# Optimization experiments

Hardware: AMD Instinct MI355X
Metric: run time of the kernel (lower is better)

## Reference

```python
import jax, jax.numpy as jnp
import numpy as np

N_EMBD = 768
N_HEAD = 12


def setup_inputs() -> dict:
    key = jax.random.key(0)
    ks = jax.random.split(key, 5)
    B, T, C = 8, 1024, N_EMBD
    s_in = 1.0 / np.sqrt(C)
    x = jax.random.normal(ks[0], (B, T, C), dtype=jnp.float32)
    w_attn = jax.random.normal(ks[1], (C, 3 * C), dtype=jnp.float32) * s_in
    b_attn = jnp.zeros((3 * C,), dtype=jnp.float32)
    w_proj = jax.random.normal(ks[2], (C, C), dtype=jnp.float32) * s_in
    b_proj = jnp.zeros((C,), dtype=jnp.float32)
    return {"x": x, "w_attn": w_attn, "b_attn": b_attn,
            "w_proj": w_proj, "b_proj": b_proj}


def reference(x, w_attn, b_attn, w_proj, b_proj):
    B, T, C = x.shape
    H, hs = N_HEAD, C // N_HEAD
    qkv = x @ w_attn + b_attn                      # [B,T,3C]
    q, k, v = jnp.split(qkv, 3, axis=-1)
    # [B,H,T,hs]
    q = q.reshape(B, T, H, hs).transpose(0, 2, 1, 3)
    k = k.reshape(B, T, H, hs).transpose(0, 2, 1, 3)
    v = v.reshape(B, T, H, hs).transpose(0, 2, 1, 3)
    att = jnp.einsum('bhqd,bhkd->bhqk', q, k) * (1.0 / np.sqrt(hs))
    causal = jnp.tril(jnp.ones((T, T), dtype=bool))
    att = jnp.where(causal, att, -jnp.inf)
    att = jax.nn.softmax(att, axis=-1)
    y = jnp.einsum('bhqk,bhkd->bhqd', att, v)      # [B,H,T,hs]
    y = y.transpose(0, 2, 1, 3).reshape(B, T, C)
    return y @ w_proj + b_proj
```

## Files before the change

kernel.cpp:

```cpp
#include <hip/hip_runtime.h>
#include <hip/hip_bf16.h>
#include <stdint.h>

typedef unsigned short u16;
typedef short short8 __attribute__((ext_vector_type(8)));
typedef short short4v __attribute__((ext_vector_type(4)));
typedef float floatx4 __attribute__((ext_vector_type(4)));

__device__ __forceinline__ float b2f(u16 v) {
  union { unsigned int u; float f; } c; c.u = ((unsigned int)v) << 16; return c.f;
}
__device__ __forceinline__ u16 f2b(float f) {
  union { float f; unsigned int u; } c; c.f = f;
  unsigned int u = c.u;
  return (u16)((u + 0x7fffu + ((u >> 16) & 1u)) >> 16);
}

__device__ __forceinline__ void gld_lds16(const u16* g, u16* l) {
  __builtin_amdgcn_global_load_lds(
      (const __attribute__((address_space(1))) unsigned int*)g,
      (__attribute__((address_space(3))) unsigned int*)l,
      16, 0, 0);
}

__device__ __forceinline__ void tile_transpose_f2b(
    const float* __restrict__ in, u16* __restrict__ out,
    int inRS, int outRS, int rb, int cb, int tid)
{
  __shared__ __align__(16) u16 t[64][72];
  const int r = tid >> 2, sg = tid & 3;
  const float* ip = in + (long)(rb + r) * inRS + cb + sg * 16;
#pragma unroll
  for (int i = 0; i < 16; i += 4) {
    float4 f = *(const float4*)(ip + i);
    t[r][sg * 16 + i]     = f2b(f.x);
    t[r][sg * 16 + i + 1] = f2b(f.y);
    t[r][sg * 16 + i + 2] = f2b(f.z);
    t[r][sg * 16 + i + 3] = f2b(f.w);
  }
  __syncthreads();
  short8 v0, v1;
#pragma unroll
  for (int i = 0; i < 8; i++) v0[i] = (short)t[sg * 16 + i][r];
#pragma unroll
  for (int i = 0; i < 8; i++) v1[i] = (short)t[sg * 16 + 8 + i][r];
  *(short8*)(out + (long)(cb + r) * outRS + rb + sg * 16)     = v0;
  *(short8*)(out + (long)(cb + r) * outRS + rb + sg * 16 + 8) = v1;
}

__global__ __launch_bounds__(256) void prep(
    const float* __restrict__ x, u16* __restrict__ xb,
    const float* __restrict__ w_attn, u16* __restrict__ wTa,
    const float* __restrict__ w_proj, u16* __restrict__ wTp)
{
  const int bid = blockIdx.x, tid = threadIdx.x;
  if (bid < 6144) {
    int i = (bid * 256 + tid) * 4;
    float4 f = *(const float4*)(x + i);
    short4v v;
    v[0] = (short)f2b(f.x); v[1] = (short)f2b(f.y);
    v[2] = (short)f2b(f.z); v[3] = (short)f2b(f.w);
    *(short4v*)(xb + i) = v;
  } else if (bid < 6576) {
    int t = bid - 6144;
    tile_transpose_f2b(w_attn, wTa, 2304, 768, (t / 36) * 64, (t % 36) * 64, tid);
  } else {
    int t = bid - 6576;
    tile_transpose_f2b(w_proj, wTp, 768, 768, (t / 12) * 64, (t % 12) * 64, tid);
  }
}

__device__ __forceinline__ void store_out(u16* p, float v)  { *p = f2b(v); }
__device__ __forceinline__ void store_out(float* p, float v) { *p = v; }

template <int BM>
__device__ __forceinline__ void stage(
    const u16* __restrict__ A, const u16* __restrict__ Bt,
    long rowbase, long colbase, int K, int k0,
    u16* dA, u16* dB, int tid)
{
  const int c0 = tid, c1 = tid + 256;
  const int ar0 = c0 >> 2, ak0 = (c0 & 3) * 8;
  const int ar1 = c1 >> 2, ak1 = (c1 & 3) * 8;
  gld_lds16(A + (rowbase + ar0) * K + k0 + ak0, dA + c0 * 8);
  if (BM == 128)
    gld_lds16(A + (rowbase + ar1) * K + k0 + ak1, dA + c1 * 8);
  gld_lds16(Bt + (colbase + ar0) * K + k0 + ak0, dB + c0 * 8);
  gld_lds16(Bt + (colbase + ar1) * K + k0 + ak1, dB + c1 * 8);
}

template <typename OT, int BM, bool SPLIT>
__global__ __launch_bounds__(256) void gemm_bt_bias(
    const u16* __restrict__ A, const u16* __restrict__ Bt,
    const float* __restrict__ bias, OT* __restrict__ C, u16* __restrict__ vT,
    int M, int N, int K, int strideC)
{
  constexpr int WNF = (BM == 128) ? 4 : 2;
  __shared__ __align__(16) u16 sA[2][BM * 32];
  __shared__ __align__(16) u16 sB[2][128 * 32];
  const int tid = threadIdx.x;
  const int lane = tid & 63;
  const int wave = tid >> 6;
  const int wm = (BM == 128) ? (wave >> 1) * 64 : 0;
  const int wn = (BM == 128) ? (wave & 1) * 64 : wave * 32;
  const int l15 = lane & 15;
  const int q = lane >> 4;
  const long rowbase = (long)blockIdx.y * BM;
  const long colbase = (long)blockIdx.x * 128;

  floatx4 acc[4][WNF];
#pragma unroll
  for (int i = 0; i < 4; i++)
#pragma unroll
    for (int j = 0; j < WNF; j++) acc[i][j] = (floatx4){0.f, 0.f, 0.f, 0.f};

  stage<BM>(A, Bt, rowbase, colbase, K, 0, sA[0], sB[0], tid);
  __syncthreads();

  const int NIT = K / 32;
  for (int it = 0; it < NIT; ++it) {
    const int cur = it & 1;
    if (it + 1 < NIT)
      stage<BM>(A, Bt, rowbase, colbase, K, (it + 1) * 32, sA[cur ^ 1], sB[cur ^ 1], tid);
    short8 af[4], bf[WNF];
#pragma unroll
    for (int mt = 0; mt < 4; mt++)
      af[mt] = *(const short8*)(sA[cur] + (wm + mt * 16 + l15) * 32 + q * 8);
#pragma unroll
    for (int nt = 0; nt < WNF; nt++)
      bf[nt] = *(const short8*)(sB[cur] + (wn + nt * 16 + l15) * 32 + q * 8);
#pragma unroll
    for (int mt = 0; mt < 4; mt++)
#pragma unroll
      for (int nt = 0; nt < WNF; nt++)
        acc[mt][nt] = __builtin_amdgcn_mfma_f32_16x16x32_bf16(af[mt], bf[nt], acc[mt][nt], 0, 0, 0);
    if (it + 1 < NIT) __syncthreads();
  }

  if (SPLIT && colbase >= 1536) {
    const long b = rowbase >> 10;
    const int t0b = (int)(rowbase & 1023) + wm;
#pragma unroll
    for (int nt = 0; nt < WNF; nt++) {
      const int col = (int)colbase + wn + nt * 16 + l15;
      const float bv = bias[col];
      const int dloc = col - 1536;
      u16* bp = vT + (b * 12 + (dloc >> 6)) * 65536L + (long)(dloc & 63) * 1024;
#pragma unroll
      for (int mt = 0; mt < 4; mt++) {
        short4v pv;
#pragma unroll
        for (int r = 0; r < 4; r++) pv[r] = (short)f2b(acc[mt][nt][r] + bv);
        *(short4v*)(bp + t0b + mt * 16 + q * 4) = pv;
      }
    }
  } else {
#pragma unroll
    for (int nt = 0; nt < WNF; nt++) {
      const long col = colbase + wn + nt * 16 + l15;
      const float bv = bias[col];
#pragma unroll
      for (int mt = 0; mt < 4; mt++)
#pragma unroll
        for (int r = 0; r < 4; r++) {
          const long row = rowbase + wm + mt * 16 + q * 4 + r;
          store_out(C + row * strideC + col, acc[mt][nt][r] + bv);
        }
    }
  }
}

#define QKV_K 768
#define QKV_NT 24
#define VMW(n) asm volatile("s_waitcnt vmcnt(" #n ")" ::: "memory")

__global__ __launch_bounds__(768, 3) void gemm_qkv_288(
    const u16* __restrict__ A, const u16* __restrict__ Bt,
    const float* __restrict__ bias, u16* __restrict__ qkOut, u16* __restrict__ vT)
{
  __shared__ __align__(16) u16 sA[4][256 * 32];
  __shared__ __align__(16) u16 sB[4][288 * 32];

  const int bid = blockIdx.x;
  const int wg = (bid & 7) * 32 + (bid >> 3);
  const int bx = wg & 7;
  const int by = wg >> 3;

  const int tid = threadIdx.x;
  const int lane = tid & 63;
  const int l15 = lane & 15, q = lane >> 4;
  const int wave = tid >> 6;
  const int wm = (wave / 6) * 128;
  const int wn = (wave % 6) * 48;
  const long rowbase = (long)by * 256;
  const long colbase = (long)bx * 288;
  const int xq = ((q ^ ((l15 >> 1) & 3)) << 3);

  const int cA0 = tid, cA1 = 768 + tid;
  const int cB0 = tid, cB1 = 768 + tid;
  const u16* pa0 = A + (rowbase + (cA0 >> 2)) * QKV_K + ((((cA0 & 3) ^ ((cA0 >> 3) & 3))) << 3);
  const u16* pa1 = A + (rowbase + (cA1 >> 2)) * QKV_K + ((((cA1 & 3) ^ ((cA1 >> 3) & 3))) << 3);
  const u16* pb0 = Bt + (colbase + (cB0 >> 2)) * QKV_K + ((((cB0 & 3) ^ ((cB0 >> 3) & 3))) << 3);
  const u16* pb1 = Bt + (colbase + (cB1 >> 2)) * QKV_K + ((((cB1 & 3) ^ ((cB1 >> 3) & 3))) << 3);
  const bool hasA1 = (tid < 256);
  const bool hasB1 = (tid < 384);

#define STAGE(t, s) do { \
    const long k0_ = (long)(t) * 32; \
    gld_lds16(pa0 + k0_, &sA[s][cA0 * 8]); \
    if (hasA1) gld_lds16(pa1 + k0_, &sA[s][cA1 * 8]); \
    gld_lds16(pb0 + k0_, &sB[s][cB0 * 8]); \
    if (hasB1) gld_lds16(pb1 + k0_, &sB[s][cB1 * 8]); } while (0)

  floatx4 acc[8][3];
#pragma unroll
  for (int i = 0; i < 8; i++)
#pragma unroll
    for (int n = 0; n < 3; n++) acc[i][n] = (floatx4){0.f, 0.f, 0.f, 0.f};

  STAGE(0, 0); STAGE(1, 1); STAGE(2, 2);
  if (wave < 4) VMW(8); else if (wave < 6) VMW(6); else VMW(4);
  __builtin_amdgcn_s_barrier();

#pragma unroll 4
  for (int j = 0; j < QKV_NT; ++j) {
    const int slot = j & 3;
    const u16* ap = sA[slot];
    const u16* bp = sB[slot];

    short8 bf[3];
#pragma unroll
    for (int nt = 0; nt < 3; nt++)
      bf[nt] = *(const short8*)(bp + (wn + nt * 16 + l15) * 32 + xq);
    short8 af[4];
#pragma unroll
    for (int mt = 0; mt < 4; mt++)
      af[mt] = *(const short8*)(ap + (wm + mt * 16 + l15) * 32 + xq);
    if (j + 3 < QKV_NT) STAGE(j + 3, (j + 3) & 3);
    __builtin_amdgcn_s_setprio(1);
#pragma unroll
    for (int mt = 0; mt < 4; mt++)
#pragma unroll
      for (int nt = 0; nt < 3; nt++)
        acc[mt][nt] = __builtin_amdgcn_mfma_f32_16x16x32_bf16(af[mt], bf[nt], acc[mt][nt], 0, 0, 0);
    __builtin_amdgcn_s_setprio(0);

#pragma unroll
    for (int mt = 0; mt < 4; mt++)
      af[mt] = *(const short8*)(ap + (wm + 64 + mt * 16 + l15) * 32 + xq);
    __builtin_amdgcn_s_setprio(1);
#pragma unroll
    for (int mt = 0; mt < 4; mt++)
#pragma unroll
      for (int nt = 0; nt < 3; nt++)
        acc[4 + mt][nt] = __builtin_amdgcn_mfma_f32_16x16x32_bf16(af[mt], bf[nt], acc[4 + mt][nt], 0, 0, 0);
    __builtin_amdgcn_s_setprio(0);

    if (j < QKV_NT - 1) {
      if (j + 3 < QKV_NT) {
        if (wave < 4) VMW(8); else if (wave < 6) VMW(6); else VMW(4);
      } else if (j + 2 < QKV_NT) {
        if (wave < 4) VMW(4); else if (wave < 6) VMW(3); else VMW(2);
      } else {
        VMW(0);
      }
      __builtin_amdgcn_s_barrier();
    }
  }
#undef STAGE

#pragma unroll
  for (int nt = 0; nt < 3; nt++) {
    const int fragc = (int)colbase + wn + nt * 16;
    const int col = fragc + l15;
    const float bv = bias[col];
    if (fragc >= 1536) {
      const long bb = rowbase >> 10;
      const int dloc = col - 1536;
      u16* op = vT + (bb * 12 + (dloc >> 6)) * 65536L + (long)(dloc & 63) * 1024;
      const int t0 = (int)(rowbase & 1023) + wm;
#pragma unroll
      for (int mt = 0; mt < 8; mt++) {
        short4v pv;
#pragma unroll
        for (int r = 0; r < 4; r++) pv[r] = (short)f2b(acc[mt][nt][r] + bv);
        *(short4v*)(op + t0 + mt * 16 + q * 4) = pv;
      }
    } else {
#pragma unroll
      for (int mt = 0; mt < 8; mt++)
#pragma unroll
        for (int r = 0; r < 4; r++) {
          const long row = rowbase + wm + mt * 16 + q * 4 + r;
          qkOut[row * 1536 + col] = f2b(acc[mt][nt][r] + bv);
        }
    }
  }
}
#undef VMW

__global__ __launch_bounds__(512) void attn_fwd(
    const u16* __restrict__ qk, const u16* __restrict__ vT, u16* __restrict__ y)
{
  const int bh = blockIdx.x;
  const int qt = 7 - blockIdx.y;
  const int b = bh / 12, h = bh % 12;
  const long rowOff = (long)b * 1024;
  const int qb = qt * 128;

  __shared__ __align__(16) u16 sK[64 * 72];
  __shared__ __align__(16) u16 sV[2][64 * 72];
  __shared__ __align__(16) u16 sP[128 * 72];

  const int tid = threadIdx.x;
  const int lane = tid & 63, wave = tid >> 6;
  const int l15 = lane & 15, q = lane >> 4;
  const int qrow_l = wave * 16 + l15;
  const int qrow_g = qb + qrow_l;
  const int wave_max_row = qb + wave * 16 + 15;

  const int sr = tid >> 3, sc = (tid & 7) * 8;
  const u16* kBase = qk + rowOff * 1536 + 768 + (long)h * 64;
  const u16* vBase = vT + (long)bh * 65536;

  short8 qf[2];
  {
    const u16* qp = qk + (long)(rowOff + qrow_g) * 1536 + h * 64 + q * 8;
    short8 a0 = *(const short8*)(qp);
    short8 a1 = *(const short8*)(qp + 32);
#pragma unroll
    for (int i = 0; i < 8; i++) {
      a0[i] = (short)f2b(b2f((u16)a0[i]) * 0.125f);
      a1[i] = (short)f2b(b2f((u16)a1[i]) * 0.125f);
    }
    qf[0] = a0; qf[1] = a1;
  }

  float m_i = -1e30f, l_i = 0.f;
  floatx4 o[4];
#pragma unroll
  for (int nt = 0; nt < 4; nt++) o[nt] = (floatx4){0.f, 0.f, 0.f, 0.f};

  const int J = 2 * qt + 1;

  *(short8*)(sK + sr * 72 + sc)    = *(const short8*)(kBase + (long)sr * 1536 + sc);
  *(short8*)(sV[0] + sr * 72 + sc) = *(const short8*)(vBase + (long)sr * 1024 + sc);
  __syncthreads();

  for (int j = 0; j <= J; j++) {
    const int jb = j * 64;
    const bool active = (jb <= wave_max_row);
    const u16* sVc = sV[j & 1];

    short8 rk = {}, rv = {};
    if (j < J) {
      rk = *(const short8*)(kBase + (long)(jb + 64 + sr) * 1536 + sc);
      rv = *(const short8*)(vBase + (long)sr * 1024 + (jb + 64) + sc);
    }

    float al = 1.f;
    if (active) {
      floatx4 sf[4];
#pragma unroll
      for (int mt = 0; mt < 4; mt++) sf[mt] = (floatx4){0.f, 0.f, 0.f, 0.f};
#pragma unroll
      for (int kk = 0; kk < 2; kk++) {
#pragma unroll
        for (int mt = 0; mt < 4; mt++) {
          short8 kf = *(const short8*)(sK + (mt * 16 + l15) * 72 + kk * 32 + q * 8);
          sf[mt] = __builtin_amdgcn_mfma_f32_16x16x32_bf16(kf, qf[kk], sf[mt], 0, 0, 0);
        }
      }

      float mx = m_i;
#pragma unroll
      for (int mt = 0; mt < 4; mt++)
#pragma unroll
        for (int r = 0; r < 4; r++) {
          int key_g = jb + mt * 16 + q * 4 + r;
          float v = sf[mt][r];
          if (key_g > qrow_g) v = -1e30f;
          sf[mt][r] = v;
          mx = fmaxf(mx, v);
        }
      mx = fmaxf(mx, __shfl_xor(mx, 16));
      mx = fmaxf(mx, __shfl_xor(mx, 32));
      al = __expf(m_i - mx);
      m_i = mx;
      float rsum = 0.f;
#pragma unroll
      for (int mt = 0; mt < 4; mt++) {
        short4v pv;
#pragma unroll
        for (int r = 0; r < 4; r++) {
          float p = __expf(sf[mt][r] - mx);
          rsum += p;
          pv[r] = (short)f2b(p);
        }
        *(short4v*)(sP + qrow_l * 72 + mt * 16 + q * 4) = pv;
      }
      rsum += __shfl_xor(rsum, 16);
      rsum += __shfl_xor(rsum, 32);
      l_i = l_i * al + rsum;
    }
    __syncthreads();

    if (j < J) {
      *(short8*)(sK + sr * 72 + sc)            = rk;
      *(short8*)(sV[(j + 1) & 1] + sr * 72 + sc) = rv;
    }

    if (active) {
      float al_r[4];
#pragma unroll
      for (int r = 0; r < 4; r++) al_r[r] = __shfl(al, q * 4 + r);
#pragma unroll
      for (int nt = 0; nt < 4; nt++)
#pragma unroll
        for (int r = 0; r < 4; r++) o[nt][r] *= al_r[r];
#pragma unroll
      for (int kk = 0; kk < 2; kk++) {
        short8 pf = *(const short8*)(sP + qrow_l * 72 + kk * 32 + q * 8);
#pragma unroll
        for (int nt = 0; nt < 4; nt++) {
          short8 vf = *(const short8*)(sVc + (nt * 16 + l15) * 72 + kk * 32 + q * 8);
          o[nt] = __builtin_amdgcn_mfma_f32_16x16x32_bf16(pf, vf, o[nt], 0, 0, 0);
        }
      }
    }
    __syncthreads();
  }

  float linv = 1.f / l_i;
  float li_r[4];
#pragma unroll
  for (int r = 0; r < 4; r++) li_r[r] = __shfl(linv, q * 4 + r);
#pragma unroll
  for (int nt = 0; nt < 4; nt++)
#pragma unroll
    for (int r = 0; r < 4; r++) {
      int row = qb + wave * 16 + q * 4 + r;
      int col = h * 64 + nt * 16 + l15;
      y[(rowOff + row) * 768 + col] = f2b(o[nt][r] * li_r[r]);
    }
}

extern "C" void kernel_launch(void* const* d_in, const int* in_sizes, int n_in,
                              void* d_out, int out_size, void* d_ws, size_t ws_size,
                              hipStream_t stream) {
  const float* x      = (const float*)d_in[0];
  const float* w_attn = (const float*)d_in[1];
  const float* b_attn = (const float*)d_in[2];
  const float* w_proj = (const float*)d_in[3];
  const float* b_proj = (const float*)d_in[4];
  float* out = (float*)d_out;

  char* ws = (char*)d_ws;
  u16* xb   = (u16*)ws; ws += (size_t)8192 * 768 * 2;
  u16* wTa  = (u16*)ws; ws += (size_t)2304 * 768 * 2;
  u16* wTp  = (u16*)ws; ws += (size_t)768 * 768 * 2;
  u16* qk   = (u16*)ws; ws += (size_t)8192 * 1536 * 2;
  u16* vT   = (u16*)ws; ws += (size_t)96 * 64 * 1024 * 2;
  u16* yatt = (u16*)ws; ws += (size_t)8192 * 768 * 2;

  prep<<<dim3(6720), 256, 0, stream>>>(x, xb, w_attn, wTa, w_proj, wTp);

  gemm_qkv_288<<<dim3(256), 768, 0, stream>>>(xb, wTa, b_attn, qk, vT);

  attn_fwd<<<dim3(96, 8), 512, 0, stream>>>(qk, vT, yatt);

  gemm_bt_bias<float, 128, false><<<dim3(6, 64), 256, 0, stream>>>(
      yatt, wTp, b_proj, out, (u16*)nullptr, 8192, 768, 768, 768);
}
```

Baseline: 188.8 us.

## Unify QKV and projection GEMMs into templated 3-stage pipelined kernel

Replaces the 256x288 QKV GEMM (768 threads, 4-stage) with a templated 128xBN kernel using 384 threads and a 3-stage cp.async-style LDS pipeline with swizzled layout. The output projection GEMM also moves from the simple double-buffered 128x128 kernel onto this pipelined kernel with 128x96 tiles and 512 blocks. The aim is better occupancy and grid fill for the QKV GEMM and better latency hiding for the projection GEMM. Smaller tiles lower data reuse per block, and the shallower pipeline may hide less memory latency.

```diff
diff --git a/kernel.cpp b/kernel.cpp
--- a/kernel.cpp
+++ b/kernel.cpp
@@ -73,116 +73,23 @@
 __device__ __forceinline__ void store_out(u16* p, float v)  { *p = f2b(v); }
 __device__ __forceinline__ void store_out(float* p, float v) { *p = v; }
 
-template <int BM>
-__device__ __forceinline__ void stage(
-    const u16* __restrict__ A, const u16* __restrict__ Bt,
-    long rowbase, long colbase, int K, int k0,
-    u16* dA, u16* dB, int tid)
-{
-  const int c0 = tid, c1 = tid + 256;
-  const int ar0 = c0 >> 2, ak0 = (c0 & 3) * 8;
-  const int ar1 = c1 >> 2, ak1 = (c1 & 3) * 8;
-  gld_lds16(A + (rowbase + ar0) * K + k0 + ak0, dA + c0 * 8);
-  if (BM == 128)
-    gld_lds16(A + (rowbase + ar1) * K + k0 + ak1, dA + c1 * 8);
-  gld_lds16(Bt + (colbase + ar0) * K + k0 + ak0, dB + c0 * 8);
-  gld_lds16(Bt + (colbase + ar1) * K + k0 + ak1, dB + c1 * 8);
-}
-
-template <typename OT, int BM, bool SPLIT>
-__global__ __launch_bounds__(256) void gemm_bt_bias(
-    const u16* __restrict__ A, const u16* __restrict__ Bt,
-    const float* __restrict__ bias, OT* __restrict__ C, u16* __restrict__ vT,
-    int M, int N, int K, int strideC)
-{
-  constexpr int WNF = (BM == 128) ? 4 : 2;
-  __shared__ __align__(16) u16 sA[2][BM * 32];
-  __shared__ __align__(16) u16 sB[2][128 * 32];
-  const int tid = threadIdx.x;
-  const int lane = tid & 63;
-  const int wave = tid >> 6;
-  const int wm = (BM == 128) ? (wave >> 1) * 64 : 0;
-  const int wn = (BM == 128) ? (wave & 1) * 64 : wave * 32;
-  const int l15 = lane & 15;
-  const int q = lane >> 4;
-  const long rowbase = (long)blockIdx.y * BM;
-  const long colbase = (long)blockIdx.x * 128;
-
-  floatx4 acc[4][WNF];
-#pragma unroll
-  for (int i = 0; i < 4; i++)
-#pragma unroll
-    for (int j = 0; j < WNF; j++) acc[i][j] = (floatx4){0.f, 0.f, 0.f, 0.f};
-
-  stage<BM>(A, Bt, rowbase, colbase, K, 0, sA[0], sB[0], tid);
-  __syncthreads();
-
-  const int NIT = K / 32;
-  for (int it = 0; it < NIT; ++it) {
-    const int cur = it & 1;
-    if (it + 1 < NIT)
-      stage<BM>(A, Bt, rowbase, colbase, K, (it + 1) * 32, sA[cur ^ 1], sB[cur ^ 1], tid);
-    short8 af[4], bf[WNF];
-#pragma unroll
-    for (int mt = 0; mt < 4; mt++)
-      af[mt] = *(const short8*)(sA[cur] + (wm + mt * 16 + l15) * 32 + q * 8);
-#pragma unroll
-    for (int nt = 0; nt < WNF; nt++)
-      bf[nt] = *(const short8*)(sB[cur] + (wn + nt * 16 + l15) * 32 + q * 8);
-#pragma unroll
-    for (int mt = 0; mt < 4; mt++)
-#pragma unroll
-      for (int nt = 0; nt < WNF; nt++)
-        acc[mt][nt] = __builtin_amdgcn_mfma_f32_16x16x32_bf16(af[mt], bf[nt], acc[mt][nt], 0, 0, 0);
-    if (it + 1 < NIT) __syncthreads();
-  }
-
-  if (SPLIT && colbase >= 1536) {
-    const long b = rowbase >> 10;
-    const int t0b = (int)(rowbase & 1023) + wm;
-#pragma unroll
-    for (int nt = 0; nt < WNF; nt++) {
-      const int col = (int)colbase + wn + nt * 16 + l15;
-      const float bv = bias[col];
-      const int dloc = col - 1536;
-      u16* bp = vT + (b * 12 + (dloc >> 6)) * 65536L + (long)(dloc & 63) * 1024;
-#pragma unroll
-      for (int mt = 0; mt < 4; mt++) {
-        short4v pv;
-#pragma unroll
-        for (int r = 0; r < 4; r++) pv[r] = (short)f2b(acc[mt][nt][r] + bv);
-        *(short4v*)(bp + t0b + mt * 16 + q * 4) = pv;
-      }
-    }
-  } else {
-#pragma unroll
-    for (int nt = 0; nt < WNF; nt++) {
-      const long col = colbase + wn + nt * 16 + l15;
-      const float bv = bias[col];
-#pragma unroll
-      for (int mt = 0; mt < 4; mt++)
-#pragma unroll
-        for (int r = 0; r < 4; r++) {
-          const long row = rowbase + wm + mt * 16 + q * 4 + r;
-          store_out(C + row * strideC + col, acc[mt][nt][r] + bv);
-        }
-    }
-  }
-}
-
 #define QKV_K 768
 #define QKV_NT 24
 #define VMW(n) asm volatile("s_waitcnt vmcnt(" #n ")" ::: "memory")
 
-__global__ __launch_bounds__(768, 3) void gemm_qkv_288(
+template <typename OT, int BN, bool SPLIT>
+__global__ __launch_bounds__(384, 3) void gemm_pipe(
     const u16* __restrict__ A, const u16* __restrict__ Bt,
-    const float* __restrict__ bias, u16* __restrict__ qkOut, u16* __restrict__ vT)
+    const float* __restrict__ bias, OT* __restrict__ C, u16* __restrict__ vT,
+    int ldc)
 {
-  __shared__ __align__(16) u16 sA[4][256 * 32];
-  __shared__ __align__(16) u16 sB[4][288 * 32];
+  constexpr int NF = BN / 48;
+  constexpr int NF1 = (NF < 3) ? NF : 3;
+  __shared__ __align__(16) u16 sA[3][128 * 32];
+  __shared__ __align__(16) u16 sB[3][BN * 32];
 
   const int bid = blockIdx.x;
-  const int wg = (bid & 7) * 32 + (bid >> 3);
+  const int wg = (bid & 7) * 64 + (bid >> 3);
   const int bx = wg & 7;
   const int by = wg >> 3;
 
@@ -190,97 +97,100 @@
   const int lane = tid & 63;
   const int l15 = lane & 15, q = lane >> 4;
   const int wave = tid >> 6;
-  const int wm = (wave / 6) * 128;
-  const int wn = (wave % 6) * 48;
-  const long rowbase = (long)by * 256;
-  const long colbase = (long)bx * 288;
+  const int wm = (wave / 3) * 64;
+  const int wn = (wave % 3) * (BN / 3);
+  const long rowbase = (long)by * 128;
+  const long colbase = (long)bx * BN;
   const int xq = ((q ^ ((l15 >> 1) & 3)) << 3);
 
-  const int cA0 = tid, cA1 = 768 + tid;
-  const int cB0 = tid, cB1 = 768 + tid;
+  const int cA0 = tid, cA1 = 384 + tid;
+  const int cB0 = tid, cB1 = 384 + tid, cB2 = 768 + tid;
+  const bool hasA1 = (tid < 128);
   const u16* pa0 = A + (rowbase + (cA0 >> 2)) * QKV_K + ((((cA0 & 3) ^ ((cA0 >> 3) & 3))) << 3);
   const u16* pa1 = A + (rowbase + (cA1 >> 2)) * QKV_K + ((((cA1 & 3) ^ ((cA1 >> 3) & 3))) << 3);
   const u16* pb0 = Bt + (colbase + (cB0 >> 2)) * QKV_K + ((((cB0 & 3) ^ ((cB0 >> 3) & 3))) << 3);
   const u16* pb1 = Bt + (colbase + (cB1 >> 2)) * QKV_K + ((((cB1 & 3) ^ ((cB1 >> 3) & 3))) << 3);
-  const bool hasA1 = (tid < 256);
-  const bool hasB1 = (tid < 384);
-
-#define STAGE(t, s) do { \
-    const long k0_ = (long)(t) * 32; \
-    gld_lds16(pa0 + k0_, &sA[s][cA0 * 8]); \
-    if (hasA1) gld_lds16(pa1 + k0_, &sA[s][cA1 * 8]); \
-    gld_lds16(pb0 + k0_, &sB[s][cB0 * 8]); \
-    if (hasB1) gld_lds16(pb1 + k0_, &sB[s][cB1 * 8]); } while (0)
-
-  floatx4 acc[8][3];
-#pragma unroll
-  for (int i = 0; i < 8; i++)
-#pragma unroll
-    for (int n = 0; n < 3; n++) acc[i][n] = (floatx4){0.f, 0.f, 0.f, 0.f};
-
-  STAGE(0, 0); STAGE(1, 1); STAGE(2, 2);
-  if (wave < 4) VMW(8); else if (wave < 6) VMW(6); else VMW(4);
+  const u16* pb2 = Bt + (colbase + (cB2 >> 2)) * QKV_K + ((((cB2 & 3) ^ ((cB2 >> 3) & 3))) << 3);
+
+  auto STAGE = [&](int t, int s) {
+    const long k0 = (long)t * 32;
+    gld_lds16(pa0 + k0, &sA[s][cA0 * 8]);
+    if (hasA1) gld_lds16(pa1 + k0, &sA[s][cA1 * 8]);
+    gld_lds16(pb0 + k0, &sB[s][cB0 * 8]);
+    if constexpr (BN == 288) {
+      gld_lds16(pb1 + k0, &sB[s][cB1 * 8]);
+      gld_lds16(pb2 + k0, &sB[s][cB2 * 8]);
+    }
+  };
+  auto WAIT_STEADY = [&]() {
+    if constexpr (BN == 288) { if (hasA1) { VMW(5); } else { VMW(4); } }
+    else                     { if (hasA1) { VMW(3); } else { VMW(2); } }
+  };
+
+  floatx4 acc[4][NF];
+#pragma unroll
+  for (int i = 0; i < 4; i++)
+#pragma unroll
+    for (int n = 0; n < NF; n++) acc[i][n] = (floatx4){0.f, 0.f, 0.f, 0.f};
+
+  STAGE(0, 0); STAGE(1, 1);
+  WAIT_STEADY();
   __builtin_amdgcn_s_barrier();
 
-#pragma unroll 4
+#pragma unroll 3
   for (int j = 0; j < QKV_NT; ++j) {
-    const int slot = j & 3;
+    const int slot = j % 3;
     const u16* ap = sA[slot];
     const u16* bp = sB[slot];
 
-    short8 bf[3];
-#pragma unroll
-    for (int nt = 0; nt < 3; nt++)
+    short8 bf[NF1], af[4];
+#pragma unroll
+    for (int nt = 0; nt < NF1; nt++)
       bf[nt] = *(const short8*)(bp + (wn + nt * 16 + l15) * 32 + xq);
-    short8 af[4];
 #pragma unroll
     for (int mt = 0; mt < 4; mt++)
       af[mt] = *(const short8*)(ap + (wm + mt * 16 + l15) * 32 + xq);
-    if (j + 3 < QKV_NT) STAGE(j + 3, (j + 3) & 3);
+    if (j + 2 < QKV_NT) STAGE(j + 2, (j + 2) % 3);
     __builtin_amdgcn_s_setprio(1);
 #pragma unroll
     for (int mt = 0; mt < 4; mt++)
 #pragma unroll
-      for (int nt = 0; nt < 3; nt++)
+      for (int nt = 0; nt < NF1; nt++)
         acc[mt][nt] = __builtin_amdgcn_mfma_f32_16x16x32_bf16(af[mt], bf[nt], acc[mt][nt], 0, 0, 0);
     __builtin_amdgcn_s_setprio(0);
 
-#pragma unroll
-    for (int mt = 0; mt < 4; mt++)
-      af[mt] = *(const short8*)(ap + (wm + 64 + mt * 16 + l15) * 32 + xq);
-    __builtin_amdgcn_s_setprio(1);
-#pragma unroll
-    for (int mt = 0; mt < 4; mt++)
+    if constexpr (NF == 6) {
 #pragma unroll
       for (int nt = 0; nt < 3; nt++)
-        acc[4 + mt][nt] = __builtin_amdgcn_mfma_f32_16x16x32_bf16(af[mt], bf[nt], acc[4 + mt][nt], 0, 0, 0);
-    __builtin_amdgcn_s_setprio(0);
+        bf[nt] = *(const short8*)(bp + (wn + 48 + nt * 16 + l15) * 32 + xq);
+      __builtin_amdgcn_s_setprio(1);
+#pragma unroll
+      for (int mt = 0; mt < 4; mt++)
+#pragma unroll
+        for (int nt = 0; nt < 3; nt++)
+          acc[mt][3 + nt] = __builtin_amdgcn_mfma_f32_16x16x32_bf16(af[mt], bf[nt], acc[mt][3 + nt], 0, 0, 0);
+      __builtin_amdgcn_s_setprio(0);
+    }
 
     if (j < QKV_NT - 1) {
-      if (j + 3 < QKV_NT) {
-        if (wave < 4) VMW(8); else if (wave < 6) VMW(6); else VMW(4);
-      } else if (j + 2 < QKV_NT) {
-        if (wave < 4) VMW(4); else if (wave < 6) VMW(3); else VMW(2);
-      } else {
-        VMW(0);
-      }
+      if (j + 2 < QKV_NT) WAIT_STEADY();
+      else                VMW(0);
       __builtin_amdgcn_s_barrier();
     }
   }
-#undef STAGE
-
-#pragma unroll
-  for (int nt = 0; nt < 3; nt++) {
+
+#pragma unroll
+  for (int nt = 0; nt < NF; nt++) {
     const int fragc = (int)colbase + wn + nt * 16;
     const int col = fragc + l15;
     const float bv = bias[col];
-    if (fragc >= 1536) {
+    if (SPLIT && fragc >= 1536) {
       const long bb = rowbase >> 10;
       const int dloc = col - 1536;
       u16* op = vT + (bb * 12 + (dloc >> 6)) * 65536L + (long)(dloc & 63) * 1024;
       const int t0 = (int)(rowbase & 1023) + wm;
 #pragma unroll
-      for (int mt = 0; mt < 8; mt++) {
+      for (int mt = 0; mt < 4; mt++) {
         short4v pv;
 #pragma unroll
         for (int r = 0; r < 4; r++) pv[r] = (short)f2b(acc[mt][nt][r] + bv);
@@ -288,11 +198,11 @@
       }
     } else {
 #pragma unroll
-      for (int mt = 0; mt < 8; mt++)
+      for (int mt = 0; mt < 4; mt++)
 #pragma unroll
         for (int r = 0; r < 4; r++) {
           const long row = rowbase + wm + mt * 16 + q * 4 + r;
-          qkOut[row * 1536 + col] = f2b(acc[mt][nt][r] + bv);
+          store_out(C + row * (long)ldc + col, acc[mt][nt][r] + bv);
         }
     }
   }
@@ -406,7 +316,7 @@
     __syncthreads();
 
     if (j < J) {
-      *(short8*)(sK + sr * 72 + sc)            = rk;
+      *(short8*)(sK + sr * 72 + sc)              = rk;
       *(short8*)(sV[(j + 1) & 1] + sr * 72 + sc) = rv;
     }
 
@@ -465,10 +375,11 @@
 
   prep<<<dim3(6720), 256, 0, stream>>>(x, xb, w_attn, wTa, w_proj, wTp);
 
-  gemm_qkv_288<<<dim3(256), 768, 0, stream>>>(xb, wTa, b_attn, qk, vT);
+  gemm_pipe<u16, 288, true><<<dim3(512), 384, 0, stream>>>(
+      xb, wTa, b_attn, qk, vT, 1536);
 
   attn_fwd<<<dim3(96, 8), 512, 0, stream>>>(qk, vT, yatt);
 
-  gemm_bt_bias<float, 128, false><<<dim3(6, 64), 256, 0, stream>>>(
-      yatt, wTp, b_proj, out, (u16*)nullptr, 8192, 768, 768, 768);
-}
+  gemm_pipe<float, 96, false><<<dim3(512), 384, 0, stream>>>(
+      yatt, wTp, b_proj, out, (u16*)nullptr, 768);
+}
```

Result: slower. 232.5 us (+23.1%).
